# Kernel optimization log

Hardware: AMD Instinct MI355X
Metric: run time of the kernel (lower is better)

The kernel has to match this reference:

```python
import jax, jax.numpy as jnp
import numpy as np

MARGIN = 1.0

def setup_inputs() -> dict:
    key = jax.random.key(0)
    k1, k2, k3 = jax.random.split(key, 3)
    B, C, D = 65536, 1000, 512
    x = jax.random.normal(k1, (B, D), dtype=jnp.float32)
    x = x / jnp.linalg.norm(x, axis=1, keepdims=True)  # docstring: ||x||2 = 1
    labels = jax.random.randint(k2, (B,), 0, C, dtype=jnp.int64)
    centers = jax.random.normal(k3, (C, D), dtype=jnp.float32)
    return {"x": x, "labels": labels, "centers": centers}

def reference(x, labels, centers):
    # l2Norm applied to the centers (module is only used when l2Norm is truthy)
    c = centers / jnp.linalg.norm(centers, axis=1, keepdims=True)  # (C, D)
    # cosine distance to every center: one batched GEMM instead of per-sample loop
    dist = 1.0 - jnp.einsum("bd,cd->bc", x, c)                      # (B, C)
    pos = jnp.take_along_axis(dist, labels[:, None], axis=1)[:, 0]  # (B,)
    # min over all classes != label: mask own class with +inf
    same = jnp.arange(c.shape[0])[None, :] == labels[:, None]       # (B, C)
    neg = jnp.min(jnp.where(same, jnp.inf, dist), axis=1)           # (B,)
    # sum of per-sample hinge losses divided by batch size == mean
    return jnp.mean(jax.nn.relu(pos + MARGIN - neg))
```

## Files before the change

kernel.cpp:

```cpp
#include <hip/hip_runtime.h>
#include <stdint.h>

typedef short v8s __attribute__((ext_vector_type(8)));
typedef short v4s __attribute__((ext_vector_type(4)));
typedef float v4f __attribute__((ext_vector_type(4)));

#define BM 128
#define BN 128
#define BK 64
#define POS_INF __builtin_inff()

typedef __attribute__((address_space(3))) unsigned int lds_uint;
typedef const __attribute__((address_space(1))) unsigned int glb_uint;

__device__ __forceinline__ void load16_lds(const void* g, void* l) {
    __builtin_amdgcn_global_load_lds((glb_uint*)g, (lds_uint*)l, 16, 0, 0);
}

__device__ __forceinline__ short f2bf(float f) {
    uint32_t u = __builtin_bit_cast(uint32_t, f);
    u += 0x7fffu + ((u >> 16) & 1u);
    return (short)(u >> 16);
}

__global__ void prep(const float* __restrict__ centers,
                     unsigned short* __restrict__ cbf,
                     int C, int D, int CP, int CB,
                     const float* __restrict__ x,
                     unsigned short* __restrict__ xbf, size_t nx,
                     int* __restrict__ cnt, int NB,
                     float* __restrict__ out) {
    const int b = blockIdx.x;
    const int t = threadIdx.x;
    if (b == 0 && t == 0) out[0] = 0.0f;
    if (b < CB) {
        const int g = b * 256 + t;
        if (g < NB) cnt[g] = 0;
        const int wave = t >> 6, lane = t & 63;
        const int row = b * 4 + wave;
        if (row >= CP) return;
        if (row >= C) {
            v4s z = {0, 0, 0, 0};
            for (int d = lane * 4; d < D; d += 256)
                *(v4s*)&cbf[(size_t)row * D + d] = z;
            return;
        }
        const float* src = centers + (size_t)row * D;
        float ss = 0.0f;
        for (int d = lane * 4; d < D; d += 256) {
            v4f f = *(const v4f*)&src[d];
            ss += f.x * f.x + f.y * f.y + f.z * f.z + f.w * f.w;
        }
        #pragma unroll
        for (int off = 32; off; off >>= 1) ss += __shfl_xor(ss, off, 64);
        const float rn = rsqrtf(ss);
        for (int d = lane * 4; d < D; d += 256) {
            v4f f = *(const v4f*)&src[d];
            v4s s;
            s.x = f2bf(f.x * rn); s.y = f2bf(f.y * rn);
            s.z = f2bf(f.z * rn); s.w = f2bf(f.w * rn);
            *(v4s*)&cbf[(size_t)row * D + d] = s;
        }
    } else {
        const size_t i = ((size_t)(b - CB) * 256 + t) * 8;
        if (i >= nx) return;
        v4f f0 = *(const v4f*)&x[i];
        v4f f1 = *(const v4f*)&x[i + 4];
        v8s s;
        s[0] = f2bf(f0.x); s[1] = f2bf(f0.y); s[2] = f2bf(f0.z); s[3] = f2bf(f0.w);
        s[4] = f2bf(f1.x); s[5] = f2bf(f1.y); s[6] = f2bf(f1.z); s[7] = f2bf(f1.w);
        *(v8s*)&xbf[i] = s;
    }
}

__global__ void gemm_fused(const float* __restrict__ xf,
                           const unsigned short* __restrict__ xbf, int useBf,
                           const unsigned short* __restrict__ cbf,
                           const int* __restrict__ labels,
                           float* __restrict__ pos, float* __restrict__ partial,
                           int* __restrict__ cnt,
                           int Bt, int C, int D, int NT, float margin,
                           float* __restrict__ out) {
    __shared__ short LDSbuf[2 * BM * BK];
    short* As = LDSbuf;
    short* Bs = LDSbuf + BM * BK;

    const int t   = threadIdx.x;
    const int bid = blockIdx.x;
    const int xcd = bid & 7;
    const int per = bid >> 3;
    const int rowblk = (per >> 3) * 8 + xcd;
    const int nt     = per & 7;
    const int row0 = rowblk * BM;
    const int n0   = nt * BN;

    const int lane = t & 63;
    const int wave = t >> 6;
    const int wm = wave >> 1, wn = wave & 1;
    const int l15 = lane & 15, q = lane >> 4;

    const int rsub = lane >> 3;
    const int csrc = (lane & 7) ^ rsub;

    v4f acc[4][4];
    #pragma unroll
    for (int i = 0; i < 4; ++i)
        #pragma unroll
        for (int j = 0; j < 4; ++j)
            acc[i][j] = (v4f){0.f, 0.f, 0.f, 0.f};

    const int KT = D / BK;
    for (int kk = 0; kk < KT; ++kk) {
        const int k0 = kk * BK;
        #pragma unroll
        for (int p = 0; p < 4; ++p) {
            const int rbase = wave * 32 + p * 8;
            const unsigned short* g =
                &cbf[(size_t)(n0 + rbase + rsub) * D + k0 + csrc * 8];
            load16_lds(g, &Bs[rbase * BK]);
        }
        if (useBf) {
            #pragma unroll
            for (int p = 0; p < 4; ++p) {
                const int rbase = wave * 32 + p * 8;
                const unsigned short* g =
                    &xbf[(size_t)(row0 + rbase + rsub) * D + k0 + csrc * 8];
                load16_lds(g, &As[rbase * BK]);
            }
        } else {
            #pragma unroll
            for (int p = 0; p < 4; ++p) {
                const int r = (t >> 3) + p * 32;
                const int cs = t & 7;
                const float* src = &xf[(size_t)(row0 + r) * D + k0 + cs * 8];
                v4f f0 = *(const v4f*)&src[0];
                v4f f1 = *(const v4f*)&src[4];
                v8s s;
                s[0] = f2bf(f0.x); s[1] = f2bf(f0.y);
                s[2] = f2bf(f0.z); s[3] = f2bf(f0.w);
                s[4] = f2bf(f1.x); s[5] = f2bf(f1.y);
                s[6] = f2bf(f1.z); s[7] = f2bf(f1.w);
                *(v8s*)&As[r * BK + (cs ^ (r & 7)) * 8] = s;
            }
        }
        __syncthreads();
        #pragma unroll
        for (int ki = 0; ki < BK; ki += 32) {
            const int cbase = ki >> 3;
            v8s a[4], b[4];
            #pragma unroll
            for (int i = 0; i < 4; ++i) {
                const int m = wm * 64 + i * 16 + l15;
                a[i] = *(const v8s*)&As[m * BK + (((cbase + q) ^ (l15 & 7)) * 8)];
            }
            #pragma unroll
            for (int j = 0; j < 4; ++j) {
                const int n = wn * 64 + j * 16 + l15;
                b[j] = *(const v8s*)&Bs[n * BK + (((cbase + q) ^ (l15 & 7)) * 8)];
            }
            #pragma unroll
            for (int i = 0; i < 4; ++i)
                #pragma unroll
                for (int j = 0; j < 4; ++j)
                    acc[i][j] = __builtin_amdgcn_mfma_f32_16x16x32_bf16(
                        a[i], b[j], acc[i][j], 0, 0, 0);
        }
        __syncthreads();
    }

    int*   Ls    = (int*)As;
    float* sMinW = (float*)Bs;
    int*   sLast = (int*)(Bs + 2 * BM * 2);
    float* wsum  = (float*)(sLast + 1);
    if (t < BM) Ls[t] = labels[row0 + t];
    __syncthreads();

    #pragma unroll
    for (int i = 0; i < 4; ++i) {
        #pragma unroll
        for (int rg = 0; rg < 4; ++rg) {
            const int row_l = wm * 64 + i * 16 + q * 4 + rg;
            const int lab = Ls[row_l];
            float m = POS_INF;
            #pragma unroll
            for (int j = 0; j < 4; ++j) {
                const int col = n0 + wn * 64 + j * 16 + l15;
                const float d = 1.0f - acc[i][j][rg];
                if (col == lab)
                    __hip_atomic_store(&pos[row0 + row_l], d,
                                       __ATOMIC_RELAXED, __HIP_MEMORY_SCOPE_AGENT);
                else if (col < C) m = fminf(m, d);
            }
            m = fminf(m, __shfl_xor(m, 1, 64));
            m = fminf(m, __shfl_xor(m, 2, 64));
            m = fminf(m, __shfl_xor(m, 4, 64));
            m = fminf(m, __shfl_xor(m, 8, 64));
            if (l15 == 0) sMinW[wn * BM + row_l] = m;
        }
    }
    __syncthreads();
    if (t < BM) {
        const float m = fminf(sMinW[t], sMinW[BM + t]);
        __hip_atomic_store(&partial[(size_t)nt * Bt + row0 + t], m,
                           __ATOMIC_RELAXED, __HIP_MEMORY_SCOPE_AGENT);
    }
    __syncthreads();

    if (t == 0) {
        __builtin_amdgcn_s_waitcnt(0);
        const int old = __hip_atomic_fetch_add(&cnt[rowblk], 1,
                                               __ATOMIC_RELAXED,
                                               __HIP_MEMORY_SCOPE_AGENT);
        *sLast = (old == NT - 1);
    }
    __syncthreads();
    if (!*sLast) return;

    float hng = 0.0f;
    if (t < BM) {
        const int r = row0 + t;
        float neg = POS_INF;
        for (int tt = 0; tt < NT; ++tt)
            neg = fminf(neg, __hip_atomic_load(&partial[(size_t)tt * Bt + r],
                                               __ATOMIC_RELAXED,
                                               __HIP_MEMORY_SCOPE_AGENT));
        const float p = __hip_atomic_load(&pos[r], __ATOMIC_RELAXED,
                                          __HIP_MEMORY_SCOPE_AGENT);
        hng = fmaxf(0.0f, p + margin - neg);
    }
    #pragma unroll
    for (int off = 32; off; off >>= 1) hng += __shfl_down(hng, off, 64);
    if (lane == 0) wsum[wave] = hng;
    __syncthreads();
    if (t == 0)
        atomicAdd(out, (wsum[0] + wsum[1] + wsum[2] + wsum[3]) * (1.0f / (float)Bt));
}

extern "C" void kernel_launch(void* const* d_in, const int* in_sizes, int n_in,
                              void* d_out, int out_size, void* d_ws, size_t ws_size,
                              hipStream_t stream) {
    const float* x       = (const float*)d_in[0];
    const int*   labels  = (const int*)d_in[1];
    const float* centers = (const float*)d_in[2];
    float* out = (float*)d_out;

    const int Bt = in_sizes[1];
    const int D  = in_sizes[0] / Bt;
    const int C  = in_sizes[2] / D;
    const int NT = (C + BN - 1) / BN;
    const int CP = NT * BN;
    const int NB = Bt / BM;

    char* ws = (char*)d_ws;
    unsigned short* cbf = (unsigned short*)ws;
    size_t off = (size_t)CP * D * 2;
    off = (off + 255) & ~(size_t)255;
    float* pos = (float*)(ws + off);      off += (size_t)Bt * 4;
    float* partial = (float*)(ws + off);  off += (size_t)NT * Bt * 4;
    int* cnt = (int*)(ws + off);          off += (size_t)NB * 4;
    off = (off + 255) & ~(size_t)255;
    unsigned short* xbf = (unsigned short*)(ws + off);
    const size_t needBig = off + (size_t)Bt * D * 2;
    const int useBf = (ws_size >= needBig) ? 1 : 0;

    const size_t nx = (size_t)Bt * D;
    const int CB = CP / 4;
    const int XB = useBf ? (int)((nx / 8 + 255) / 256) : 0;
    prep<<<CB + XB, 256, 0, stream>>>(centers, cbf, C, D, CP, CB, x, xbf, nx,
                                      cnt, NB, out);

    gemm_fused<<<NB * NT, 256, 0, stream>>>(x, xbf, useBf, cbf, labels, pos,
                                            partial, cnt, Bt, C, D, NT, 1.0f, out);
}
```

Measured before the change: 292.6 us.

## Enlarge row tile to 256 with 512-thread blocks and always use bf16 x

Doubles the batch-row tile to 256 rows per block and moves to 8 waves (512 threads), so each center tile loaded into LDS is reused across more rows and the block count halves. The fallback path that converted fp32 x to bf16 inside the GEMM is removed, so the bf16 copy of x is always produced and read. Labels are now loaded before the K loop to hide their latency. The change assumes the workspace is always large enough for the bf16 x buffer, and the epilogue's shared-memory offsets and wave indexing must still match the larger tile.

```diff
diff --git a/kernel.cpp b/kernel.cpp
--- a/kernel.cpp
+++ b/kernel.cpp
@@ -5,7 +5,7 @@
 typedef short v4s __attribute__((ext_vector_type(4)));
 typedef float v4f __attribute__((ext_vector_type(4)));
 
-#define BM 128
+#define BM 256
 #define BN 128
 #define BK 64
 #define POS_INF __builtin_inff()
@@ -73,15 +73,15 @@
     }
 }
 
-__global__ void gemm_fused(const float* __restrict__ xf,
-                           const unsigned short* __restrict__ xbf, int useBf,
-                           const unsigned short* __restrict__ cbf,
-                           const int* __restrict__ labels,
-                           float* __restrict__ pos, float* __restrict__ partial,
-                           int* __restrict__ cnt,
-                           int Bt, int C, int D, int NT, float margin,
-                           float* __restrict__ out) {
-    __shared__ short LDSbuf[2 * BM * BK];
+__global__ void __launch_bounds__(512)
+gemm_fused(const unsigned short* __restrict__ xbf,
+           const unsigned short* __restrict__ cbf,
+           const int* __restrict__ labels,
+           float* __restrict__ pos, float* __restrict__ partial,
+           int* __restrict__ cnt,
+           int Bt, int C, int D, int NT, float margin,
+           float* __restrict__ out) {
+    __shared__ short LDSbuf[(BM + BN) * BK];
     short* As = LDSbuf;
     short* Bs = LDSbuf + BM * BK;
 
@@ -96,11 +96,15 @@
 
     const int lane = t & 63;
     const int wave = t >> 6;
-    const int wm = wave >> 1, wn = wave & 1;
+    const int wm = wave >> 1;
+    const int wn = wave & 1;
     const int l15 = lane & 15, q = lane >> 4;
 
     const int rsub = lane >> 3;
     const int csrc = (lane & 7) ^ rsub;
+
+    int myLab = 0;
+    if (t < BM) myLab = labels[row0 + t];
 
     v4f acc[4][4];
     #pragma unroll
@@ -116,32 +120,15 @@
         for (int p = 0; p < 4; ++p) {
             const int rbase = wave * 32 + p * 8;
             const unsigned short* g =
+                &xbf[(size_t)(row0 + rbase + rsub) * D + k0 + csrc * 8];
+            load16_lds(g, &As[rbase * BK]);
+        }
+        #pragma unroll
+        for (int p = 0; p < 2; ++p) {
+            const int rbase = wave * 16 + p * 8;
+            const unsigned short* g =
                 &cbf[(size_t)(n0 + rbase + rsub) * D + k0 + csrc * 8];
             load16_lds(g, &Bs[rbase * BK]);
-        }
-        if (useBf) {
-            #pragma unroll
-            for (int p = 0; p < 4; ++p) {
-                const int rbase = wave * 32 + p * 8;
-                const unsigned short* g =
-                    &xbf[(size_t)(row0 + rbase + rsub) * D + k0 + csrc * 8];
-                load16_lds(g, &As[rbase * BK]);
-            }
-        } else {
-            #pragma unroll
-            for (int p = 0; p < 4; ++p) {
-                const int r = (t >> 3) + p * 32;
-                const int cs = t & 7;
-                const float* src = &xf[(size_t)(row0 + r) * D + k0 + cs * 8];
-                v4f f0 = *(const v4f*)&src[0];
-                v4f f1 = *(const v4f*)&src[4];
-                v8s s;
-                s[0] = f2bf(f0.x); s[1] = f2bf(f0.y);
-                s[2] = f2bf(f0.z); s[3] = f2bf(f0.w);
-                s[4] = f2bf(f1.x); s[5] = f2bf(f1.y);
-                s[6] = f2bf(f1.z); s[7] = f2bf(f1.w);
-                *(v8s*)&As[r * BK + (cs ^ (r & 7)) * 8] = s;
-            }
         }
         __syncthreads();
         #pragma unroll
@@ -172,7 +159,7 @@
     float* sMinW = (float*)Bs;
     int*   sLast = (int*)(Bs + 2 * BM * 2);
     float* wsum  = (float*)(sLast + 1);
-    if (t < BM) Ls[t] = labels[row0 + t];
+    if (t < BM) Ls[t] = myLab;
     __syncthreads();
 
     #pragma unroll
@@ -232,8 +219,12 @@
     for (int off = 32; off; off >>= 1) hng += __shfl_down(hng, off, 64);
     if (lane == 0) wsum[wave] = hng;
     __syncthreads();
-    if (t == 0)
-        atomicAdd(out, (wsum[0] + wsum[1] + wsum[2] + wsum[3]) * (1.0f / (float)Bt));
+    if (t == 0) {
+        float s = 0.0f;
+        #pragma unroll
+        for (int w = 0; w < 8; ++w) s += wsum[w];
+        atomicAdd(out, s * (1.0f / (float)Bt));
+    }
 }
 
 extern "C" void kernel_launch(void* const* d_in, const int* in_sizes, int n_in,
@@ -260,15 +251,13 @@
     int* cnt = (int*)(ws + off);          off += (size_t)NB * 4;
     off = (off + 255) & ~(size_t)255;
     unsigned short* xbf = (unsigned short*)(ws + off);
-    const size_t needBig = off + (size_t)Bt * D * 2;
-    const int useBf = (ws_size >= needBig) ? 1 : 0;
 
     const size_t nx = (size_t)Bt * D;
     const int CB = CP / 4;
-    const int XB = useBf ? (int)((nx / 8 + 255) / 256) : 0;
+    const int XB = (int)((nx / 8 + 255) / 256);
     prep<<<CB + XB, 256, 0, stream>>>(centers, cbf, C, D, CP, CB, x, xbf, nx,
                                       cnt, NB, out);
 
-    gemm_fused<<<NB * NT, 256, 0, stream>>>(x, xbf, useBf, cbf, labels, pos,
-                                            partial, cnt, Bt, C, D, NT, 1.0f, out);
-}
+    gemm_fused<<<NB * NT, 512, 0, stream>>>(xbf, cbf, labels, pos, partial, cnt,
+                                            Bt, C, D, NT, 1.0f, out);
+}
```

Result: no change. 290.2 us (-0.8%).
